# Optimization experiments

Measured on AMD Instinct MI355X. Metric: run time of the kernel, lower is better.

## Reference

```python
import jax, jax.numpy as jnp
import numpy as np

GROUPS = 32
EPS = 1e-6  # flax.linen.GroupNorm default


def group_norm(x, scale, bias):
    B, H, W, C = x.shape
    xg = x.reshape(B, H, W, GROUPS, C // GROUPS)
    mean = jnp.mean(xg, axis=(1, 2, 4), keepdims=True)
    var = jnp.var(xg, axis=(1, 2, 4), keepdims=True)
    xn = (xg - mean) * jax.lax.rsqrt(var + EPS)
    return xn.reshape(B, H, W, C) * scale + bias


def setup_inputs() -> dict:
    key = jax.random.key(0)
    ks = jax.random.split(key, 8)
    B, H, W, C = 8, 64, 64, 128
    s = C ** -0.5  # fan-in style init scale for 1x1 conv kernels
    return {
        "x": jax.random.normal(ks[0], (B, H, W, C), dtype=jnp.float32),
        "gn_scale": jnp.ones((C,), dtype=jnp.float32),
        "gn_bias": jnp.zeros((C,), dtype=jnp.float32),
        "wq": jax.random.normal(ks[1], (C, C), dtype=jnp.float32) * s,
        "bq": jnp.zeros((C,), dtype=jnp.float32),
        "wk": jax.random.normal(ks[2], (C, C), dtype=jnp.float32) * s,
        "bk": jnp.zeros((C,), dtype=jnp.float32),
        "wv": jax.random.normal(ks[3], (C, C), dtype=jnp.float32) * s,
        "bv": jnp.zeros((C,), dtype=jnp.float32),
        "wo": jax.random.normal(ks[4], (C, C), dtype=jnp.float32) * s,
        "bo": jnp.zeros((C,), dtype=jnp.float32),
    }


def reference(x, gn_scale, gn_bias, wq, bq, wk, bk, wv, bv, wo, bo):
    B, H, W, C = x.shape
    N = H * W
    h = group_norm(x, gn_scale, gn_bias)                       # [B,H,W,C]
    hf = h.reshape(B, N, C)
    q = hf @ wq + bq                                           # 1x1 conv == per-position matmul
    k = hf @ wk + bk
    v = hf @ wv + bv
    w_ = jnp.einsum('bqd,bkd->bqk', q, k) * (C ** -0.5)        # [B,N,N] full score matrix
    w_ = jax.nn.softmax(w_, axis=2)
    o = jnp.einsum('bqk,bkd->bqd', w_, v)                      # [B,N,C]
    o = o @ wo + bo
    return x + o.reshape(B, H, W, C)
```

## Files before the change

### kernel.cpp

```cpp
#include <hip/hip_runtime.h>
#include <hip/hip_bf16.h>

#define NN 4096
#define CC 128
#define SCALE 0.088388347648318447f
#define LOG2E 1.4426950408889634f

typedef __attribute__((ext_vector_type(8))) short short8v;
typedef __attribute__((ext_vector_type(4))) float f32x4;
typedef __attribute__((ext_vector_type(16))) float f32x16;

#define Z16 {0.f,0.f,0.f,0.f,0.f,0.f,0.f,0.f,0.f,0.f,0.f,0.f,0.f,0.f,0.f,0.f}

__device__ __forceinline__ short f2bf(float f) {
  unsigned u = __float_as_uint(f);
  u = (u + 0x7FFFu + ((u >> 16) & 1u)) >> 16;
  return (short)u;
}
__device__ __forceinline__ float bf2f(short s) {
  return __uint_as_float(((unsigned)(unsigned short)s) << 16);
}
__device__ __forceinline__ unsigned pk2bf(float lo, float hi) {
  unsigned r;
  asm("v_cvt_pk_bf16_f32 %0, %1, %2" : "=v"(r) : "v"(lo), "v"(hi));
  return r;
}
__device__ __forceinline__ f32x4 mfma16(short8v a, short8v b, f32x4 c) {
  return __builtin_amdgcn_mfma_f32_16x16x32_bf16(a, b, c, 0, 0, 0);
}
__device__ __forceinline__ f32x16 mfma32(short8v a, short8v b, f32x16 c) {
  return __builtin_amdgcn_mfma_f32_32x32x16_bf16(a, b, c, 0, 0, 0);
}
__device__ __forceinline__ void gload16(const void* g, void* l) {
  __builtin_amdgcn_global_load_lds(
      (const __attribute__((address_space(1))) unsigned*)g,
      (__attribute__((address_space(3))) unsigned*)l, 16, 0, 0);
}

__global__ __launch_bounds__(256) void prep_k(
    const float* __restrict__ x,
    const float* __restrict__ wq, const float* __restrict__ wk,
    const float* __restrict__ wv, const float* __restrict__ wo,
    const float* __restrict__ bq, short* __restrict__ wT,
    float* __restrict__ bqs, float* __restrict__ macc,
    float* __restrict__ vacc) {
  if (blockIdx.x >= 256) {
    int gid = (blockIdx.x - 256) * 256 + threadIdx.x;
    int widx = gid >> 14, e = gid & 16383;
    int kk = e >> 7, n = e & 127;
    const float* src = (widx == 0) ? wq : (widx == 1) ? wk
                     : (widx == 2) ? wv : wo;
    float v = src[kk * 128 + n];
    if (widx == 0) v *= SCALE * LOG2E;
    wT[widx * 16384 + n * 128 + kk] = f2bf(v);
    if (gid < 128) bqs[gid] = bq[gid] * SCALE * LOG2E;
    return;
  }
  int b = blockIdx.x >> 5, rc = blockIdx.x & 31;
  const float4* xp = reinterpret_cast<const float4*>(
      x + (size_t)b * NN * CC + (size_t)rc * 128 * CC);
  int tid = threadIdx.x;
  float s = 0.f, ss = 0.f;
  #pragma unroll
  for (int j = 0; j < 16; ++j) {
    float4 v = xp[tid + 256 * j];
    s  += v.x + v.y + v.z + v.w;
    ss += v.x * v.x + v.y * v.y + v.z * v.z + v.w * v.w;
  }
  __shared__ float as_[256], ass_[256];
  as_[tid] = s; ass_[tid] = ss;
  __syncthreads();
  if (tid < 32) {
    float ts = 0.f, tss = 0.f;
    #pragma unroll
    for (int j = 0; j < 8; ++j) { ts += as_[tid + 32 * j]; tss += ass_[tid + 32 * j]; }
    atomicAdd(&macc[b * 32 + tid], ts);
    atomicAdd(&vacc[b * 32 + tid], tss);
  }
}

__global__ __launch_bounds__(256) void fqkv_k(
    const float* __restrict__ x, const float* __restrict__ macc,
    const float* __restrict__ vacc, const float* __restrict__ gsc,
    const float* __restrict__ gbi, const short* __restrict__ wT,
    const float* __restrict__ bqs, const float* __restrict__ bk,
    const float* __restrict__ bv, short* __restrict__ qout,
    short* __restrict__ kout, short* __restrict__ vtout) {
  __shared__ short wlds[128][136];
  int lane = threadIdx.x & 63, wid = threadIdx.x >> 6;
  int row0 = blockIdx.x * 64 + wid * 16;
  int arow = row0 + (lane & 15);
  int q4 = lane >> 4;
  int bidx = arow >> 12;
  short8v a[4];
  #pragma unroll
  for (int dt = 0; dt < 4; ++dt) {
    int c0 = dt * 32 + q4 * 8;
    float4 v0 = *reinterpret_cast<const float4*>(x + (size_t)arow * CC + c0);
    float4 v1 = *reinterpret_cast<const float4*>(x + (size_t)arow * CC + c0 + 4);
    int g0 = bidx * 32 + (c0 >> 2);
    float mu0 = macc[g0] * (1.f / 16384.f);
    float r0 = rsqrtf(vacc[g0] * (1.f / 16384.f) - mu0 * mu0 + 1e-6f);
    float mu1 = macc[g0 + 1] * (1.f / 16384.f);
    float r1 = rsqrtf(vacc[g0 + 1] * (1.f / 16384.f) - mu1 * mu1 + 1e-6f);
    float4 s0 = *reinterpret_cast<const float4*>(gsc + c0);
    float4 s1 = *reinterpret_cast<const float4*>(gsc + c0 + 4);
    float4 b0 = *reinterpret_cast<const float4*>(gbi + c0);
    float4 b1 = *reinterpret_cast<const float4*>(gbi + c0 + 4);
    union { short s[8]; short8v v; } pk;
    pk.s[0] = f2bf((v0.x - mu0) * r0 * s0.x + b0.x);
    pk.s[1] = f2bf((v0.y - mu0) * r0 * s0.y + b0.y);
    pk.s[2] = f2bf((v0.z - mu0) * r0 * s0.z + b0.z);
    pk.s[3] = f2bf((v0.w - mu0) * r0 * s0.w + b0.w);
    pk.s[4] = f2bf((v1.x - mu1) * r1 * s1.x + b1.x);
    pk.s[5] = f2bf((v1.y - mu1) * r1 * s1.y + b1.y);
    pk.s[6] = f2bf((v1.z - mu1) * r1 * s1.z + b1.z);
    pk.s[7] = f2bf((v1.w - mu1) * r1 * s1.w + b1.w);
    a[dt] = pk.v;
  }
  for (int ph = 0; ph < 3; ++ph) {
    if (ph) __syncthreads();
    const short* w = wT + ph * 16384;
    for (int i = threadIdx.x; i < 2048; i += 256) {
      int n = i >> 4, kk = (i & 15) << 3;
      *reinterpret_cast<short8v*>(&wlds[n][kk]) =
          *reinterpret_cast<const short8v*>(w + n * 128 + kk);
    }
    __syncthreads();
    const float* bias = (ph == 0) ? bqs : (ph == 1) ? bk : bv;
    f32x4 zero = {0.f, 0.f, 0.f, 0.f};
    f32x4 acc[8];
    #pragma unroll
    for (int nt = 0; nt < 8; ++nt) acc[nt] = zero;
    #pragma unroll
    for (int nt = 0; nt < 8; ++nt) {
      #pragma unroll
      for (int kk = 0; kk < 4; ++kk) {
        short8v b = *reinterpret_cast<const short8v*>(
            &wlds[nt * 16 + (lane & 15)][kk * 32 + q4 * 8]);
        acc[nt] = mfma16(a[kk], b, acc[nt]);
      }
    }
    short* dst = (ph == 0) ? qout : (ph == 1) ? kout : vtout;
    #pragma unroll
    for (int nt = 0; nt < 8; ++nt) {
      #pragma unroll
      for (int r = 0; r < 4; ++r) {
        int row = row0 + q4 * 4 + r;
        int col = nt * 16 + (lane & 15);
        float v = acc[nt][r] + bias[col];
        if (ph == 2) {
          int b_ = row >> 12, n = row & 4095;
          dst[((size_t)b_ * 128 + col) * 4096 + n] = f2bf(v);
        } else {
          dst[(size_t)row * 128 + col] = f2bf(v);
        }
      }
    }
  }
}

template <int S>
__global__ __launch_bounds__(256, 3) void attn5_k(
    const short* __restrict__ q, const short* __restrict__ k,
    const short* __restrict__ vt, short* __restrict__ opart,
    float* __restrict__ ls) {
  constexpr int KVLEN = NN / S;
  constexpr int NIT = KVLEN / 32;
  __shared__ short8v smem_v[2048];
  char* smem = (char*)smem_v;
  const int tid = threadIdx.x;
  const int lane = tid & 63, warp = tid >> 6;
  const int hh = lane >> 5, ql = lane & 31;
  const int split = (int)blockIdx.x % S;
  const int qb_lin = (int)blockIdx.x / S;
  const int b = qb_lin >> 5, qblk = qb_lin & 31;
  const int kv0 = split * KVLEN;

  const size_t bqko = (size_t)b * NN * CC;
  short8v qf[8];
  {
    int qrow = qblk * 128 + warp * 32 + ql;
    const short* qp = q + bqko + (size_t)qrow * CC + hh * 8;
    #pragma unroll
    for (int dc = 0; dc < 8; ++dc)
      qf[dc] = *reinterpret_cast<const short8v*>(qp + dc * 16);
  }
  const char* kg = (const char*)(k + bqko);
  const char* vg = (const char*)(vt + (size_t)b * CC * NN);

  auto stage = [&](int buf, int it) {
    const int kvo = kv0 + it * 32;
    char* base = smem + buf * 16384;
    #pragma unroll
    for (int p = 0; p < 2; ++p) {
      int c = p * 256 + warp * 64 + lane;
      int krow = c >> 4, kj = c & 15;
      gload16(kg + (size_t)(kvo + krow) * 256 + 16 * (kj ^ (krow & 7)),
              base + p * 4096 + warp * 1024);
      int vd = c >> 2, vj = c & 3;
      gload16(vg + (size_t)vd * (NN * 2) + (size_t)kvo * 2 +
                  16 * (vj ^ ((vd >> 1) & 3)),
              base + 8192 + p * 4096 + warp * 1024);
    }
  };

  f32x16 oacc[4] = {Z16, Z16, Z16, Z16};
  float l_run = 0.f;

  stage(0, 0);
  asm volatile("s_waitcnt vmcnt(0)" ::: "memory");
  __builtin_amdgcn_s_barrier();

  const int swzK = (ql & 7) << 4;
  const int swzV = (ql & 6) << 3;
  for (int it = 0; it < NIT; ++it) {
    const int cur = it & 1;
    if (it + 1 < NIT) stage(cur ^ 1, it + 1);

    const char* kr_p = smem + cur * 16384 + ql * 256;
    f32x16 sT = Z16;
    #pragma unroll
    for (int dc = 0; dc < 8; ++dc) {
      short8v kf = *reinterpret_cast<const short8v*>(
          kr_p + ((32 * dc + 16 * hh) ^ swzK));
      sT = mfma32(kf, qf[dc], sT);
    }

    float rsum = 0.f;
    #pragma unroll
    for (int r = 0; r < 16; ++r) {
      float p = exp2f(sT[r]);
      sT[r] = p; rsum += p;
    }
    l_run += rsum;

    const char* vb_ = smem + cur * 16384 + 8192;
    #pragma unroll
    for (int st = 0; st < 2; ++st) {
      union { unsigned u[4]; short8v v; } pu;
      #pragma unroll
      for (int w = 0; w < 4; ++w)
        pu.u[w] = pk2bf(sT[8 * st + 2 * w], sT[8 * st + 2 * w + 1]);
      const int o1 = (32 * st + 8 * hh) ^ swzV;
      const int o2 = (32 * st + 8 * hh + 16) ^ swzV;
      #pragma unroll
      for (int dt = 0; dt < 4; ++dt) {
        const char* vr_p = vb_ + (32 * dt + ql) * 64;
        union { unsigned long long d[2]; short8v v; } vf;
        vf.d[0] = *reinterpret_cast<const unsigned long long*>(vr_p + o1);
        vf.d[1] = *reinterpret_cast<const unsigned long long*>(vr_p + o2);
        oacc[dt] = mfma32(pu.v, vf.v, oacc[dt]);
      }
    }

    asm volatile("s_waitcnt vmcnt(0)" ::: "memory");
    __builtin_amdgcn_s_barrier();
  }

  l_run += __shfl_xor(l_run, 32);
  float rinv = 1.f / l_run;
  short* op = opart + ((size_t)(split * 8 + b) * NN + qblk * 128 + warp * 32) * CC;
  #pragma unroll
  for (int r = 0; r < 16; ++r) {
    int qp = (r & 3) + 8 * (r >> 2) + 4 * hh;
    float ri = __shfl(rinv, qp);
    #pragma unroll
    for (int dt = 0; dt < 4; ++dt)
      op[(size_t)qp * CC + 32 * dt + ql] = f2bf(oacc[dt][r] * ri);
  }
  if (hh == 0) {
    size_t ix = (size_t)(split * 8 + b) * NN + qblk * 128 + warp * 32 + ql;
    ls[ix] = l_run;
  }
}

template <int S>
__global__ __launch_bounds__(256) void projoc_k(const short* __restrict__ opart,
    const float* __restrict__ ls, const short* __restrict__ wT,
    const float* __restrict__ bias, const float* __restrict__ x,
    float* __restrict__ out) {
  __shared__ short wlds[128][136];
  int lane = threadIdx.x & 63, wid = threadIdx.x >> 6;
  for (int i = threadIdx.x; i < 2048; i += 256) {
    int n = i >> 4, kk = (i & 15) << 3;
    *reinterpret_cast<short8v*>(&wlds[n][kk]) =
        *reinterpret_cast<const short8v*>(wT + n * 128 + kk);
  }
  int row0 = blockIdx.x * 64 + wid * 16;
  int arow = row0 + (lane & 15);
  int q4 = lane >> 4;
  float wgt[S];
  {
    float tot = 0.f;
    #pragma unroll
    for (int s = 0; s < S; ++s) {
      wgt[s] = ls[(size_t)s * 32768 + arow];
      tot += wgt[s];
    }
    float inv = 1.f / tot;
    #pragma unroll
    for (int s = 0; s < S; ++s) wgt[s] *= inv;
  }
  short8v a[4];
  #pragma unroll
  for (int dt = 0; dt < 4; ++dt) {
    int c0 = dt * 32 + q4 * 8;
    float acc8[8] = {0.f, 0.f, 0.f, 0.f, 0.f, 0.f, 0.f, 0.f};
    #pragma unroll
    for (int s = 0; s < S; ++s) {
      short8v v = *reinterpret_cast<const short8v*>(
          opart + ((size_t)s * 32768 + arow) * CC + c0);
      #pragma unroll
      for (int e = 0; e < 8; ++e) acc8[e] += wgt[s] * bf2f(v[e]);
    }
    union { short s[8]; short8v v; } pk;
    #pragma unroll
    for (int e = 0; e < 8; ++e) pk.s[e] = f2bf(acc8[e]);
    a[dt] = pk.v;
  }
  __syncthreads();
  f32x4 zero = {0.f, 0.f, 0.f, 0.f};
  f32x4 acc[8];
  #pragma unroll
  for (int nt = 0; nt < 8; ++nt) acc[nt] = zero;
  #pragma unroll
  for (int nt = 0; nt < 8; ++nt) {
    #pragma unroll
    for (int kk = 0; kk < 4; ++kk) {
      short8v b = *reinterpret_cast<const short8v*>(
          &wlds[nt * 16 + (lane & 15)][kk * 32 + q4 * 8]);
      acc[nt] = mfma16(a[kk], b, acc[nt]);
    }
  }
  #pragma unroll
  for (int nt = 0; nt < 8; ++nt) {
    #pragma unroll
    for (int r = 0; r < 4; ++r) {
      int row = row0 + q4 * 4 + r;
      int col = nt * 16 + (lane & 15);
      out[(size_t)row * 128 + col] =
          acc[nt][r] + bias[col] + x[(size_t)row * 128 + col];
    }
  }
}

extern "C" void kernel_launch(void* const* d_in, const int* in_sizes, int n_in,
                              void* d_out, int out_size, void* d_ws, size_t ws_size,
                              hipStream_t stream) {
  (void)in_sizes; (void)n_in; (void)out_size;
  const float* x   = (const float*)d_in[0];
  const float* gsc = (const float*)d_in[1];
  const float* gbi = (const float*)d_in[2];
  const float* wq  = (const float*)d_in[3];
  const float* bq  = (const float*)d_in[4];
  const float* wk  = (const float*)d_in[5];
  const float* bk  = (const float*)d_in[6];
  const float* wv  = (const float*)d_in[7];
  const float* bv  = (const float*)d_in[8];
  const float* wo  = (const float*)d_in[9];
  const float* bo  = (const float*)d_in[10];
  float* out = (float*)d_out;

  char* ws = (char*)d_ws;
  constexpr size_t OFF_WT   = 0;
  constexpr size_t OFF_BQS  = 131072;
  constexpr size_t OFF_MACC = 131584;
  constexpr size_t OFF_VACC = 132608;
  constexpr size_t OFF_QB   = 133632;
  constexpr size_t OFF_KB   = OFF_QB + 8388608;
  constexpr size_t OFF_VT   = OFF_KB + 8388608;
  constexpr size_t OFF_OP   = OFF_VT + 8388608;
  constexpr size_t NEED4 = OFF_OP + 4 * 8388608 + 4 * 131072;
  constexpr size_t NEED2 = OFF_OP + 2 * 8388608 + 2 * 131072;

  short* wT   = (short*)(ws + OFF_WT);
  float* bqs  = (float*)(ws + OFF_BQS);
  float* macc = (float*)(ws + OFF_MACC);
  float* vacc = (float*)(ws + OFF_VACC);
  short* qb   = (short*)(ws + OFF_QB);
  short* kb   = (short*)(ws + OFF_KB);
  short* vtb  = (short*)(ws + OFF_VT);
  short* opart= (short*)(ws + OFF_OP);
  const int S = (ws_size >= NEED4) ? 4 : (ws_size >= NEED2) ? 2 : 1;
  float* ls = (float*)(ws + OFF_OP + (size_t)S * 8388608);

  hipMemsetAsync(ws + OFF_MACC, 0, 2048, stream);
  prep_k<<<512, 256, 0, stream>>>(x, wq, wk, wv, wo, bq, wT, bqs, macc, vacc);
  fqkv_k<<<512, 256, 0, stream>>>(x, macc, vacc, gsc, gbi, wT, bqs, bk, bv,
                                  qb, kb, vtb);
  if (S == 4) {
    attn5_k<4><<<1024, 256, 0, stream>>>(qb, kb, vtb, opart, ls);
    projoc_k<4><<<512, 256, 0, stream>>>(opart, ls, wT + 49152, bo, x, out);
  } else if (S == 2) {
    attn5_k<2><<<512, 256, 0, stream>>>(qb, kb, vtb, opart, ls);
    projoc_k<2><<<512, 256, 0, stream>>>(opart, ls, wT + 49152, bo, x, out);
  } else {
    attn5_k<1><<<256, 256, 0, stream>>>(qb, kb, vtb, opart, ls);
    projoc_k<1><<<512, 256, 0, stream>>>(opart, ls, wT + 49152, bo, x, out);
  }
}
```

Measured before the change: 131.7 us.

## Deepen attention KV pipeline to four buffers and overlap QK with PV

The attention kernel moves from double to quad-buffered LDS staging, keeping three K/V tiles in flight with partial vmcnt waits. It also software-pipelines the loop so the next tile's QK^T MFMAs are issued alongside the current tile's exp and PV. V^T is written with a permuted sequence index so each PV operand becomes one contiguous 16-byte LDS read instead of two swizzled 8-byte reads. LDS doubles and launch bounds drop to 2 blocks per CU, trading occupancy for more latency hiding.

Result: no change. 131.4 us (-0.2%).

```diff
diff --git a/kernel.cpp b/kernel.cpp
--- a/kernel.cpp
+++ b/kernel.cpp
@@ -151,7 +151,8 @@
         float v = acc[nt][r] + bias[col];
         if (ph == 2) {
           int b_ = row >> 12, n = row & 4095;
-          dst[((size_t)b_ * 128 + col) * 4096 + n] = f2bf(v);
+          int np = (n & ~12) | ((n & 4) << 1) | ((n & 8) >> 1);
+          dst[((size_t)b_ * 128 + col) * 4096 + np] = f2bf(v);
         } else {
           dst[(size_t)row * 128 + col] = f2bf(v);
         }
@@ -161,13 +162,13 @@
 }
 
 template <int S>
-__global__ __launch_bounds__(256, 3) void attn5_k(
+__global__ __launch_bounds__(256, 2) void attn6_k(
     const short* __restrict__ q, const short* __restrict__ k,
     const short* __restrict__ vt, short* __restrict__ opart,
     float* __restrict__ ls) {
   constexpr int KVLEN = NN / S;
   constexpr int NIT = KVLEN / 32;
-  __shared__ short8v smem_v[2048];
+  __shared__ short8v smem_v[4096];
   char* smem = (char*)smem_v;
   const int tid = threadIdx.x;
   const int lane = tid & 63, warp = tid >> 6;
@@ -198,64 +199,69 @@
       int krow = c >> 4, kj = c & 15;
       gload16(kg + (size_t)(kvo + krow) * 256 + 16 * (kj ^ (krow & 7)),
               base + p * 4096 + warp * 1024);
-      int vd = c >> 2, vj = c & 3;
-      gload16(vg + (size_t)vd * (NN * 2) + (size_t)kvo * 2 +
-                  16 * (vj ^ ((vd >> 1) & 3)),
+      gload16(vg + (size_t)(c & 127) * (NN * 2) + (size_t)kvo * 2 +
+                  16 * (c >> 7),
               base + 8192 + p * 4096 + warp * 1024);
     }
   };
 
-  f32x16 oacc[4] = {Z16, Z16, Z16, Z16};
-  float l_run = 0.f;
-
-  stage(0, 0);
-  asm volatile("s_waitcnt vmcnt(0)" ::: "memory");
-  __builtin_amdgcn_s_barrier();
-
   const int swzK = (ql & 7) << 4;
-  const int swzV = (ql & 6) << 3;
-  for (int it = 0; it < NIT; ++it) {
-    const int cur = it & 1;
-    if (it + 1 < NIT) stage(cur ^ 1, it + 1);
-
-    const char* kr_p = smem + cur * 16384 + ql * 256;
-    f32x16 sT = Z16;
+  auto qk = [&](const char* kbase) -> f32x16 {
+    const char* kr_p = kbase + ql * 256;
+    f32x16 s = Z16;
     #pragma unroll
     for (int dc = 0; dc < 8; ++dc) {
       short8v kf = *reinterpret_cast<const short8v*>(
           kr_p + ((32 * dc + 16 * hh) ^ swzK));
-      sT = mfma32(kf, qf[dc], sT);
-    }
+      s = mfma32(kf, qf[dc], s);
+    }
+    return s;
+  };
+
+  f32x16 oacc[4] = {Z16, Z16, Z16, Z16};
+  float l_run = 0.f;
+
+  stage(0, 0);
+  if (NIT > 1) stage(1, 1);
+  if (NIT > 2) stage(2, 2);
+  asm volatile("s_waitcnt vmcnt(4)" ::: "memory");
+  __builtin_amdgcn_s_barrier();
+
+  f32x16 sA = qk(smem);
+
+  #pragma unroll 4
+  for (int it = 0; it < NIT; ++it) {
+    const int cb = it & 3, nb = (it + 1) & 3, pb = (it + 3) & 3;
+    stage(pb, (it + 3 < NIT) ? it + 3 : NIT - 1);
 
     float rsum = 0.f;
     #pragma unroll
     for (int r = 0; r < 16; ++r) {
-      float p = exp2f(sT[r]);
-      sT[r] = p; rsum += p;
+      float p = exp2f(sA[r]);
+      sA[r] = p; rsum += p;
     }
     l_run += rsum;
 
-    const char* vb_ = smem + cur * 16384 + 8192;
+    f32x16 sB = qk(smem + nb * 16384);
+
+    const char* vb_ = smem + cb * 16384 + 8192;
     #pragma unroll
     for (int st = 0; st < 2; ++st) {
       union { unsigned u[4]; short8v v; } pu;
       #pragma unroll
       for (int w = 0; w < 4; ++w)
-        pu.u[w] = pk2bf(sT[8 * st + 2 * w], sT[8 * st + 2 * w + 1]);
-      const int o1 = (32 * st + 8 * hh) ^ swzV;
-      const int o2 = (32 * st + 8 * hh + 16) ^ swzV;
+        pu.u[w] = pk2bf(sA[8 * st + 2 * w], sA[8 * st + 2 * w + 1]);
+      const char* vr_p = vb_ + (2 * st + hh) * 2048 + ql * 16;
       #pragma unroll
       for (int dt = 0; dt < 4; ++dt) {
-        const char* vr_p = vb_ + (32 * dt + ql) * 64;
-        union { unsigned long long d[2]; short8v v; } vf;
-        vf.d[0] = *reinterpret_cast<const unsigned long long*>(vr_p + o1);
-        vf.d[1] = *reinterpret_cast<const unsigned long long*>(vr_p + o2);
-        oacc[dt] = mfma32(pu.v, vf.v, oacc[dt]);
+        short8v vf = *reinterpret_cast<const short8v*>(vr_p + dt * 512);
+        oacc[dt] = mfma32(pu.v, vf, oacc[dt]);
       }
     }
 
-    asm volatile("s_waitcnt vmcnt(0)" ::: "memory");
+    asm volatile("s_waitcnt vmcnt(4)" ::: "memory");
     __builtin_amdgcn_s_barrier();
+    sA = sB;
   }
 
   l_run += __shfl_xor(l_run, 32);
@@ -390,13 +396,13 @@
   fqkv_k<<<512, 256, 0, stream>>>(x, macc, vacc, gsc, gbi, wT, bqs, bk, bv,
                                   qb, kb, vtb);
   if (S == 4) {
-    attn5_k<4><<<1024, 256, 0, stream>>>(qb, kb, vtb, opart, ls);
+    attn6_k<4><<<1024, 256, 0, stream>>>(qb, kb, vtb, opart, ls);
     projoc_k<4><<<512, 256, 0, stream>>>(opart, ls, wT + 49152, bo, x, out);
   } else if (S == 2) {
-    attn5_k<2><<<512, 256, 0, stream>>>(qb, kb, vtb, opart, ls);
+    attn6_k<2><<<512, 256, 0, stream>>>(qb, kb, vtb, opart, ls);
     projoc_k<2><<<512, 256, 0, stream>>>(opart, ls, wT + 49152, bo, x, out);
   } else {
-    attn5_k<1><<<256, 256, 0, stream>>>(qb, kb, vtb, opart, ls);
+    attn6_k<1><<<256, 256, 0, stream>>>(qb, kb, vtb, opart, ls);
     projoc_k<1><<<512, 256, 0, stream>>>(opart, ls, wT + 49152, bo, x, out);
   }
 }
```

## Process two query tiles per block to reuse staged K/V and permute V layout

Applied to the files above, without the earlier changes.

Each attention block now handles 256 query rows (two 128-row tiles) so every K/V tile staged in LDS feeds twice as many MFMAs, halving global K/V traffic per query. The V-transpose writer permutes sequence indices so the attention kernel can read V fragments with a single 16-byte LDS load instead of two swizzled 8-byte loads. The cost is more registers (two Q fragment sets, two accumulator sets), occupancy hint lowered from 3 to 2 waves per SIMD, and half as many blocks in the grid.

New measurement: 132.1 us. Within noise of the previous version (+0.3%).

```diff
diff --git a/kernel.cpp b/kernel.cpp
--- a/kernel.cpp
+++ b/kernel.cpp
@@ -151,7 +151,8 @@
         float v = acc[nt][r] + bias[col];
         if (ph == 2) {
           int b_ = row >> 12, n = row & 4095;
-          dst[((size_t)b_ * 128 + col) * 4096 + n] = f2bf(v);
+          int np = (n & ~12) | ((n & 4) << 1) | ((n & 8) >> 1);
+          dst[((size_t)b_ * 128 + col) * 4096 + np] = f2bf(v);
         } else {
           dst[(size_t)row * 128 + col] = f2bf(v);
         }
@@ -161,7 +162,7 @@
 }
 
 template <int S>
-__global__ __launch_bounds__(256, 3) void attn5_k(
+__global__ __launch_bounds__(256, 2) void attn7_k(
     const short* __restrict__ q, const short* __restrict__ k,
     const short* __restrict__ vt, short* __restrict__ opart,
     float* __restrict__ ls) {
@@ -174,17 +175,19 @@
   const int hh = lane >> 5, ql = lane & 31;
   const int split = (int)blockIdx.x % S;
   const int qb_lin = (int)blockIdx.x / S;
-  const int b = qb_lin >> 5, qblk = qb_lin & 31;
+  const int b = qb_lin >> 4, qblk = qb_lin & 15;
   const int kv0 = split * KVLEN;
 
   const size_t bqko = (size_t)b * NN * CC;
-  short8v qf[8];
+  short8v qf0[8], qf1[8];
   {
-    int qrow = qblk * 128 + warp * 32 + ql;
+    int qrow = qblk * 256 + warp * 32 + ql;
     const short* qp = q + bqko + (size_t)qrow * CC + hh * 8;
     #pragma unroll
-    for (int dc = 0; dc < 8; ++dc)
-      qf[dc] = *reinterpret_cast<const short8v*>(qp + dc * 16);
+    for (int dc = 0; dc < 8; ++dc) {
+      qf0[dc] = *reinterpret_cast<const short8v*>(qp + dc * 16);
+      qf1[dc] = *reinterpret_cast<const short8v*>(qp + 128 * CC + dc * 16);
+    }
   }
   const char* kg = (const char*)(k + bqko);
   const char* vg = (const char*)(vt + (size_t)b * CC * NN);
@@ -198,59 +201,77 @@
       int krow = c >> 4, kj = c & 15;
       gload16(kg + (size_t)(kvo + krow) * 256 + 16 * (kj ^ (krow & 7)),
               base + p * 4096 + warp * 1024);
-      int vd = c >> 2, vj = c & 3;
-      gload16(vg + (size_t)vd * (NN * 2) + (size_t)kvo * 2 +
-                  16 * (vj ^ ((vd >> 1) & 3)),
+      gload16(vg + (size_t)(c & 127) * (NN * 2) + (size_t)kvo * 2 +
+                  16 * (c >> 7),
               base + 8192 + p * 4096 + warp * 1024);
     }
   };
 
-  f32x16 oacc[4] = {Z16, Z16, Z16, Z16};
-  float l_run = 0.f;
+  f32x16 oacc0[4] = {Z16, Z16, Z16, Z16};
+  f32x16 oacc1[4] = {Z16, Z16, Z16, Z16};
+  float l0 = 0.f, l1 = 0.f;
 
   stage(0, 0);
   asm volatile("s_waitcnt vmcnt(0)" ::: "memory");
   __builtin_amdgcn_s_barrier();
 
   const int swzK = (ql & 7) << 4;
-  const int swzV = (ql & 6) << 3;
   for (int it = 0; it < NIT; ++it) {
     const int cur = it & 1;
     if (it + 1 < NIT) stage(cur ^ 1, it + 1);
 
     const char* kr_p = smem + cur * 16384 + ql * 256;
-    f32x16 sT = Z16;
+    f32x16 sT0 = Z16, sT1 = Z16;
     #pragma unroll
     for (int dc = 0; dc < 8; ++dc) {
       short8v kf = *reinterpret_cast<const short8v*>(
           kr_p + ((32 * dc + 16 * hh) ^ swzK));
-      sT = mfma32(kf, qf[dc], sT);
-    }
-
-    float rsum = 0.f;
-    #pragma unroll
-    for (int r = 0; r < 16; ++r) {
-      float p = exp2f(sT[r]);
-      sT[r] = p; rsum += p;
-    }
-    l_run += rsum;
+      sT0 = mfma32(kf, qf0[dc], sT0);
+      sT1 = mfma32(kf, qf1[dc], sT1);
+    }
+
+    unsigned pu0[2][4], pu1[2][4];
+    {
+      float rs = 0.f;
+      #pragma unroll
+      for (int r = 0; r < 16; ++r) {
+        float p = exp2f(sT0[r]);
+        sT0[r] = p; rs += p;
+      }
+      l0 += rs;
+      #pragma unroll
+      for (int st = 0; st < 2; ++st)
+        #pragma unroll
+        for (int w = 0; w < 4; ++w)
+          pu0[st][w] = pk2bf(sT0[8 * st + 2 * w], sT0[8 * st + 2 * w + 1]);
+    }
+    {
+      float rs = 0.f;
+      #pragma unroll
+      for (int r = 0; r < 16; ++r) {
+        float p = exp2f(sT1[r]);
+        sT1[r] = p; rs += p;
+      }
+      l1 += rs;
+      #pragma unroll
+      for (int st = 0; st < 2; ++st)
+        #pragma unroll
+        for (int w = 0; w < 4; ++w)
+          pu1[st][w] = pk2bf(sT1[8 * st + 2 * w], sT1[8 * st + 2 * w + 1]);
+    }
 
     const char* vb_ = smem + cur * 16384 + 8192;
     #pragma unroll
     for (int st = 0; st < 2; ++st) {
-      union { unsigned u[4]; short8v v; } pu;
-      #pragma unroll
-      for (int w = 0; w < 4; ++w)
-        pu.u[w] = pk2bf(sT[8 * st + 2 * w], sT[8 * st + 2 * w + 1]);
-      const int o1 = (32 * st + 8 * hh) ^ swzV;
-      const int o2 = (32 * st + 8 * hh + 16) ^ swzV;
+      union { unsigned u[4]; short8v v; } a0, a1;
+      #pragma unroll
+      for (int w = 0; w < 4; ++w) { a0.u[w] = pu0[st][w]; a1.u[w] = pu1[st][w]; }
+      const char* vr_p = vb_ + (2 * st + hh) * 2048 + ql * 16;
       #pragma unroll
       for (int dt = 0; dt < 4; ++dt) {
-        const char* vr_p = vb_ + (32 * dt + ql) * 64;
-        union { unsigned long long d[2]; short8v v; } vf;
-        vf.d[0] = *reinterpret_cast<const unsigned long long*>(vr_p + o1);
-        vf.d[1] = *reinterpret_cast<const unsigned long long*>(vr_p + o2);
-        oacc[dt] = mfma32(pu.v, vf.v, oacc[dt]);
+        short8v vf = *reinterpret_cast<const short8v*>(vr_p + dt * 512);
+        oacc0[dt] = mfma32(a0.v, vf, oacc0[dt]);
+        oacc1[dt] = mfma32(a1.v, vf, oacc1[dt]);
       }
     }
 
@@ -258,20 +279,25 @@
     __builtin_amdgcn_s_barrier();
   }
 
-  l_run += __shfl_xor(l_run, 32);
-  float rinv = 1.f / l_run;
-  short* op = opart + ((size_t)(split * 8 + b) * NN + qblk * 128 + warp * 32) * CC;
+  l0 += __shfl_xor(l0, 32);
+  l1 += __shfl_xor(l1, 32);
+  float ri0 = 1.f / l0, ri1 = 1.f / l1;
+  size_t row0 = (size_t)(split * 8 + b) * NN + qblk * 256 + warp * 32;
+  short* op = opart + row0 * CC;
   #pragma unroll
   for (int r = 0; r < 16; ++r) {
     int qp = (r & 3) + 8 * (r >> 2) + 4 * hh;
-    float ri = __shfl(rinv, qp);
-    #pragma unroll
-    for (int dt = 0; dt < 4; ++dt)
-      op[(size_t)qp * CC + 32 * dt + ql] = f2bf(oacc[dt][r] * ri);
+    float ra = __shfl(ri0, qp);
+    float rb = __shfl(ri1, qp);
+    #pragma unroll
+    for (int dt = 0; dt < 4; ++dt) {
+      op[(size_t)qp * CC + 32 * dt + ql] = f2bf(oacc0[dt][r] * ra);
+      op[(size_t)(qp + 128) * CC + 32 * dt + ql] = f2bf(oacc1[dt][r] * rb);
+    }
   }
   if (hh == 0) {
-    size_t ix = (size_t)(split * 8 + b) * NN + qblk * 128 + warp * 32 + ql;
-    ls[ix] = l_run;
+    ls[row0 + ql] = l0;
+    ls[row0 + 128 + ql] = l1;
   }
 }
 
@@ -390,13 +416,13 @@
   fqkv_k<<<512, 256, 0, stream>>>(x, macc, vacc, gsc, gbi, wT, bqs, bk, bv,
                                   qb, kb, vtb);
   if (S == 4) {
-    attn5_k<4><<<1024, 256, 0, stream>>>(qb, kb, vtb, opart, ls);
+    attn7_k<4><<<512, 256, 0, stream>>>(qb, kb, vtb, opart, ls);
     projoc_k<4><<<512, 256, 0, stream>>>(opart, ls, wT + 49152, bo, x, out);
   } else if (S == 2) {
-    attn5_k<2><<<512, 256, 0, stream>>>(qb, kb, vtb, opart, ls);
+    attn7_k<2><<<256, 256, 0, stream>>>(qb, kb, vtb, opart, ls);
     projoc_k<2><<<512, 256, 0, stream>>>(opart, ls, wT + 49152, bo, x, out);
   } else {
-    attn5_k<1><<<256, 256, 0, stream>>>(qb, kb, vtb, opart, ls);
+    attn7_k<1><<<128, 256, 0, stream>>>(qb, kb, vtb, opart, ls);
     projoc_k<1><<<512, 256, 0, stream>>>(opart, ls, wT + 49152, bo, x, out);
   }
 }
```
